# Kernel tuning notes

Hardware: AMD Instinct MI355X
Metric: run time of the kernel (lower is better)

Reference implementation:

```python
import jax, jax.numpy as jnp
import numpy as np

N = 50000
E = 800000
F_IN = 256
HID = 96
N_CLS = 32
NEG_SLOPE = 0.2


def setup_inputs() -> dict:
    key = jax.random.key(0)
    ks = jax.random.split(key, 10)
    x = jax.random.normal(ks[0], (N, F_IN), dtype=jnp.float32)
    edge_index = jax.random.randint(ks[1], (2, E), 0, N, dtype=jnp.int64)
    s1 = 1.0 / np.sqrt(F_IN)
    s2 = 1.0 / np.sqrt(HID)
    return {
        "x": x,
        "edge_index": edge_index,
        "W1": jax.random.normal(ks[2], (F_IN, HID), dtype=jnp.float32) * s1,
        "a1_src": jax.random.normal(ks[3], (HID,), dtype=jnp.float32) * s2,
        "a1_dst": jax.random.normal(ks[4], (HID,), dtype=jnp.float32) * s2,
        "b1": jnp.zeros((HID,), dtype=jnp.float32),
        "W2": jax.random.normal(ks[5], (HID, N_CLS), dtype=jnp.float32) * s2,
        "a2_src": jax.random.normal(ks[6], (N_CLS,), dtype=jnp.float32) * (1.0 / np.sqrt(N_CLS)),
        "a2_dst": jax.random.normal(ks[7], (N_CLS,), dtype=jnp.float32) * (1.0 / np.sqrt(N_CLS)),
        "b2": jnp.zeros((N_CLS,), dtype=jnp.float32),
    }


def _gat_conv(x, src, dst, W, a_src, a_dst, b, n_nodes):
    # single-head GATConv (PyG defaults), self-loops already in src/dst
    h = x @ W                                  # [N, out]
    alpha_src = h @ a_src                      # [N]
    alpha_dst = h @ a_dst                      # [N]
    e = alpha_src[src] + alpha_dst[dst]        # [E'] edge logits (msg j->i: dst groups)
    e = jnp.where(e > 0, e, NEG_SLOPE * e)     # leaky_relu
    # segment softmax over edges grouped by destination node
    m = jax.ops.segment_max(e, dst, num_segments=n_nodes)
    ex = jnp.exp(e - m[dst])
    denom = jax.ops.segment_sum(ex, dst, num_segments=n_nodes)
    alpha = ex / denom[dst]                    # [E']
    out = jax.ops.segment_sum(alpha[:, None] * h[src], dst, num_segments=n_nodes)
    return out + b


def reference(x, edge_index, W1, a1_src, a1_dst, b1, W2, a2_src, a2_dst, b2):
    loops = jnp.arange(N, dtype=edge_index.dtype)
    src = jnp.concatenate([edge_index[0], loops])
    dst = jnp.concatenate([edge_index[1], loops])
    h = _gat_conv(x, src, dst, W1, a1_src, a1_dst, b1, N)
    h = jax.nn.elu(h)
    # dropout omitted (eval mode, training=False)
    out = _gat_conv(h, src, dst, W2, a2_src, a2_dst, b2, N)
    return jax.nn.log_softmax(out, axis=1)
```

## Files before the change

kernel.cpp:

```cpp
#include <hip/hip_runtime.h>
#include <cstdint>
#include <cstddef>

#define NNODES 50000
#define NEDGES 800000
#define MEDGES (NEDGES + NNODES)
#define FIN    256
#define HID    96
#define NCLS   32
#define NEG_SLOPE 0.2f

#define NBUCK  391
#define BCAP   3072

typedef unsigned int uint32;
typedef __attribute__((ext_vector_type(8))) short short8;
typedef __attribute__((ext_vector_type(4))) float f32x4;

__device__ __forceinline__ ushort bf_round(float f) {
    uint32 u = __float_as_uint(f);
    u += 0x7FFFu + ((u >> 16) & 1u);
    return (ushort)(u >> 16);
}
__device__ __forceinline__ uint32 pack_bf16x2(float a, float b) {
    return (uint32)bf_round(a) | ((uint32)bf_round(b) << 16);
}
__device__ __forceinline__ float bf_lo(uint32 u) { return __uint_as_float(u << 16); }
__device__ __forceinline__ float bf_hi(uint32 u) { return __uint_as_float(u & 0xFFFF0000u); }
__device__ __forceinline__ float lrelu(float t) { return (t > 0.f) ? t : NEG_SLOPE * t; }
__device__ __forceinline__ float af(int i) { return __int_as_float(i); }
__device__ __forceinline__ float elu_fast(float t) { return (t > 0.f) ? t : (__expf(t) - 1.f); }


__global__ __launch_bounds__(256) void bucket1_kernel(const int* __restrict__ ei,
                                                      int* __restrict__ gcount,
                                                      int* __restrict__ staging) {
    __shared__ int hist[NBUCK];
    __shared__ int base_sh[NBUCK];
    for (int i = threadIdx.x; i < NBUCK; i += 256) hist[i] = 0;
    __syncthreads();

    int v[8], rk[8], bk[8];
    int e0 = blockIdx.x * 2048;
#pragma unroll
    for (int i = 0; i < 8; ++i) {
        int e = e0 + i * 256 + threadIdx.x;
        if (e < MEDGES) {
            int s, d;
            if (e < NEDGES) { s = ei[e]; d = ei[NEDGES + e]; }
            else            { s = e - NEDGES; d = s; }
            bk[i] = d >> 7;
            v[i]  = s | ((d & 127) << 16);
            rk[i] = atomicAdd(&hist[bk[i]], 1);
        } else bk[i] = -1;
    }
    __syncthreads();
    for (int i = threadIdx.x; i < NBUCK; i += 256) {
        int c = hist[i];
        base_sh[i] = c ? atomicAdd(&gcount[i], c) : 0;
    }
    __syncthreads();
#pragma unroll
    for (int i = 0; i < 8; ++i) {
        if (bk[i] >= 0) {
            int pos = base_sh[bk[i]] + rk[i];
            if (pos < BCAP)
                staging[(size_t)bk[i] * BCAP + pos] = v[i];
        }
    }
}

__global__ __launch_bounds__(256) void bucket2_kernel(const int* __restrict__ staging,
                                                      const int* __restrict__ gcount,
                                                      int* __restrict__ rowptr,
                                                      int* __restrict__ esrc) {
    __shared__ int dcount[128];
    __shared__ int dincl[128];
    __shared__ int dexcl[128];
    __shared__ int fillc[128];
    __shared__ int red_s[256];

    const int b = blockIdx.x;
    const int t = threadIdx.x;

    int pv = 0;
    for (int idx = t; idx < b; idx += 256) pv += gcount[idx];
    red_s[t] = pv;
    __syncthreads();
    for (int off2 = 128; off2; off2 >>= 1) {
        if (t < off2) red_s[t] += red_s[t + off2];
        __syncthreads();
    }
    const int ebase = red_s[0];
    const int cnt   = gcount[b];
    const int node0 = b << 7;
    const int* st   = staging + (size_t)b * BCAP;

    for (int i = t; i < 128; i += 256) { dcount[i] = 0; fillc[i] = 0; }
    __syncthreads();

    for (int i = t; i < cnt; i += 256)
        atomicAdd(&dcount[st[i] >> 16], 1);
    __syncthreads();

    if (t < 128) dincl[t] = dcount[t];
    __syncthreads();
    for (int off = 1; off < 128; off <<= 1) {
        int val = (t >= off && t < 128) ? dincl[t - off] : 0;
        __syncthreads();
        if (t < 128) dincl[t] += val;
        __syncthreads();
    }
    if (t < 128) {
        int excl = dincl[t] - dcount[t];
        dexcl[t] = excl;
        int node = node0 + t;
        if (node < NNODES) rowptr[node] = ebase + excl;
    }
    if (b == NBUCK - 1 && t == 0) rowptr[NNODES] = MEDGES;
    __syncthreads();

    for (int i = t; i < cnt; i += 256) {
        int v = st[i];
        int dd = v >> 16;
        int r = atomicAdd(&fillc[dd], 1);
        esrc[ebase + dexcl[dd] + r] = v & 0xFFFF;
    }
}


__global__ __launch_bounds__(256) void packw_kernel(const float* __restrict__ W1,
                                                    const float* __restrict__ W2,
                                                    ushort* __restrict__ W1p,
                                                    ushort* __restrict__ W2p,
                                                    int* __restrict__ gcount) {
    int stride = gridDim.x * 256;
    for (int idx = blockIdx.x * 256 + threadIdx.x; idx < NBUCK; idx += stride)
        gcount[idx] = 0;
    for (int idx = blockIdx.x * 256 + threadIdx.x; idx < 6 * 8 * 64 * 8; idx += stride) {
        int j     = idx & 7;
        int lane  = (idx >> 3) & 63;
        int kstep = (idx >> 9) & 7;
        int ntile = idx >> 12;
        int k = kstep * 32 + ((lane >> 4) << 3) + j;
        int n = ntile * 16 + (lane & 15);
        W1p[idx] = bf_round(W1[(size_t)k * 96 + n]);
    }
    for (int idx = blockIdx.x * 256 + threadIdx.x; idx < 2 * 3 * 64 * 8; idx += stride) {
        int j     = idx & 7;
        int lane  = (idx >> 3) & 63;
        int kstep = (idx >> 9) % 3;
        int ntile = (idx >> 9) / 3;
        int k = kstep * 32 + ((lane >> 4) << 3) + j;
        int n = ntile * 16 + (lane & 15);
        W2p[idx] = bf_round(W2[(size_t)k * 32 + n]);
    }
}


__global__ __launch_bounds__(256) void gemm1_kernel(const float* __restrict__ x,
                                                    const ushort* __restrict__ W1p,
                                                    const float* __restrict__ a_src,
                                                    const float* __restrict__ a_dst,
                                                    ushort* __restrict__ h1,
                                                    float* __restrict__ as1,
                                                    float* __restrict__ ad1) {
    const int tid  = threadIdx.x;
    const int lane = tid & 63;
    const int wv   = tid >> 6;
    const int m    = lane & 15;
    const int quad = lane >> 4;
    const int node0 = blockIdx.x * 64;

    int arow = node0 + wv * 16 + m;
    if (arow >= NNODES) arow = NNODES - 1;
    const float* xr = x + (size_t)arow * FIN + quad * 8;

    const short8* Wp = (const short8*)W1p;

    f32x4 acc[6];
#pragma unroll
    for (int t = 0; t < 6; ++t) acc[t] = (f32x4){0.f, 0.f, 0.f, 0.f};

#pragma unroll
    for (int ks = 0; ks < 8; ++ks) {
        float4 v0 = *(const float4*)(xr + ks * 32);
        float4 v1 = *(const float4*)(xr + ks * 32 + 4);
        short8 a;
        a[0] = (short)bf_round(v0.x); a[1] = (short)bf_round(v0.y);
        a[2] = (short)bf_round(v0.z); a[3] = (short)bf_round(v0.w);
        a[4] = (short)bf_round(v1.x); a[5] = (short)bf_round(v1.y);
        a[6] = (short)bf_round(v1.z); a[7] = (short)bf_round(v1.w);
#pragma unroll
        for (int t = 0; t < 6; ++t) {
            short8 b = Wp[(t * 8 + ks) * 64 + lane];
            acc[t] = __builtin_amdgcn_mfma_f32_16x16x32_bf16(a, b, acc[t], 0, 0, 0);
        }
    }

    float as_reg[6], ad_reg[6];
#pragma unroll
    for (int t = 0; t < 6; ++t) {
        as_reg[t] = a_src[t * 16 + m];
        ad_reg[t] = a_dst[t * 16 + m];
    }

#pragma unroll
    for (int r = 0; r < 4; ++r) {
        int node = node0 + wv * 16 + quad * 4 + r;
        float ps = 0.f, pd = 0.f;
#pragma unroll
        for (int t = 0; t < 6; ++t) {
            ps += acc[t][r] * as_reg[t];
            pd += acc[t][r] * ad_reg[t];
        }
#pragma unroll
        for (int off = 1; off < 16; off <<= 1) {
            ps += __shfl_xor(ps, off);
            pd += __shfl_xor(pd, off);
        }
        if (node < NNODES) {
            ushort* hp = h1 + (size_t)node * 96 + m;
#pragma unroll
            for (int t = 0; t < 6; ++t) hp[t * 16] = bf_round(acc[t][r]);
            if (m == 0) { as1[node] = ps; ad1[node] = pd; }
        }
    }
}


__global__ __launch_bounds__(256) void gemm2_kernel(const uint32* __restrict__ y48,
                                                    const ushort* __restrict__ W2p,
                                                    const float* __restrict__ a_src,
                                                    const float* __restrict__ a_dst,
                                                    uint32* __restrict__ h2b,
                                                    float* __restrict__ as2,
                                                    float* __restrict__ ad2) {
    const int tid  = threadIdx.x;
    const int lane = tid & 63;
    const int wv   = tid >> 6;
    const int m    = lane & 15;
    const int quad = lane >> 4;
    const int node0 = blockIdx.x * 64;

    int arow = node0 + wv * 16 + m;
    if (arow >= NNODES) arow = NNODES - 1;
    const short8* Ar = (const short8*)(y48 + (size_t)arow * 48);
    const short8* Wp = (const short8*)W2p;

    f32x4 acc[2];
    acc[0] = (f32x4){0.f, 0.f, 0.f, 0.f};
    acc[1] = (f32x4){0.f, 0.f, 0.f, 0.f};

#pragma unroll
    for (int ks = 0; ks < 3; ++ks) {
        short8 a = Ar[ks * 4 + quad];
#pragma unroll
        for (int t = 0; t < 2; ++t) {
            short8 b = Wp[(t * 3 + ks) * 64 + lane];
            acc[t] = __builtin_amdgcn_mfma_f32_16x16x32_bf16(a, b, acc[t], 0, 0, 0);
        }
    }

    float as_reg[2], ad_reg[2];
#pragma unroll
    for (int t = 0; t < 2; ++t) {
        as_reg[t] = a_src[t * 16 + m];
        ad_reg[t] = a_dst[t * 16 + m];
    }

#pragma unroll
    for (int r = 0; r < 4; ++r) {
        int node = node0 + wv * 16 + quad * 4 + r;
        float ps = 0.f, pd = 0.f;
#pragma unroll
        for (int t = 0; t < 2; ++t) {
            ps += acc[t][r] * as_reg[t];
            pd += acc[t][r] * ad_reg[t];
        }
#pragma unroll
        for (int off = 1; off < 16; off <<= 1) {
            ps += __shfl_xor(ps, off);
            pd += __shfl_xor(pd, off);
        }
        if (node < NNODES) {
            h2b[(size_t)node * 16 + m] = pack_bf16x2(acc[0][r], acc[1][r]);
            if (m == 0) { as2[node] = ps; ad2[node] = pd; }
        }
    }
}


__global__ __launch_bounds__(256) void agg96_kernel(const ushort* __restrict__ h,
                                                    const float* __restrict__ asrc,
                                                    const float* __restrict__ adst,
                                                    const float* __restrict__ bias,
                                                    const int* __restrict__ rowptr,
                                                    const int* __restrict__ esrc,
                                                    uint32* __restrict__ out1b) {
    __shared__ int2 sa[4][2][32];
    const int wave = threadIdx.x >> 6;
    const int lane = threadIdx.x & 63;
    const int hf   = lane >> 5;
    const int fl32 = lane & 31;
    const int i = blockIdx.x * 8 + wave * 2 + hf;

    const int start = rowptr[i];
    const int deg   = rowptr[i + 1] - start;
    const float ad  = adst[i];
    const int fl    = (fl32 < 24) ? fl32 : 23;

    float acc0 = 0.f, acc1 = 0.f, acc2 = 0.f, acc3 = 0.f;

    if (deg <= 32) {
        bool valid = fl32 < deg;
        int s_reg = valid ? esrc[start + fl32] : 0;
        float e = valid ? lrelu(asrc[s_reg] + ad) : -1e30f;
        float mx = e;
#pragma unroll
        for (int off = 16; off; off >>= 1) mx = fmaxf(mx, __shfl_xor(mx, off));
        float ex = valid ? __expf(e - mx) : 0.f;
        float sum = ex;
#pragma unroll
        for (int off = 16; off; off >>= 1) sum += __shfl_xor(sum, off);
        sa[wave][hf][fl32] = make_int2(s_reg, __float_as_int(ex / sum));

        const int4* sap = (const int4*)&sa[wave][hf][0];

        for (int eb = 0; eb < deg; eb += 8) {
            int4 qa = sap[(eb >> 1) + 0];
            int4 qb = sap[(eb >> 1) + 1];
            int4 qc = sap[(eb >> 1) + 2];
            int4 qd = sap[(eb >> 1) + 3];
            const uint2* r0 = (const uint2*)(h + (size_t)qa.x * 96);
            const uint2* r1 = (const uint2*)(h + (size_t)qa.z * 96);
            const uint2* r2 = (const uint2*)(h + (size_t)qb.x * 96);
            const uint2* r3 = (const uint2*)(h + (size_t)qb.z * 96);
            const uint2* r4 = (const uint2*)(h + (size_t)qc.x * 96);
            const uint2* r5 = (const uint2*)(h + (size_t)qc.z * 96);
            const uint2* r6 = (const uint2*)(h + (size_t)qd.x * 96);
            const uint2* r7 = (const uint2*)(h + (size_t)qd.z * 96);
            uint2 u0 = r0[fl], u1 = r1[fl], u2 = r2[fl], u3 = r3[fl];
            uint2 u4 = r4[fl], u5 = r5[fl], u6 = r6[fl], u7 = r7[fl];
            float a0 = af(qa.y), a1 = af(qa.w), a2 = af(qb.y), a3 = af(qb.w);
            float a4 = af(qc.y), a5 = af(qc.w), a6 = af(qd.y), a7 = af(qd.w);
            acc0 += a0 * bf_lo(u0.x) + a1 * bf_lo(u1.x) + a2 * bf_lo(u2.x) + a3 * bf_lo(u3.x)
                  + a4 * bf_lo(u4.x) + a5 * bf_lo(u5.x) + a6 * bf_lo(u6.x) + a7 * bf_lo(u7.x);
            acc1 += a0 * bf_hi(u0.x) + a1 * bf_hi(u1.x) + a2 * bf_hi(u2.x) + a3 * bf_hi(u3.x)
                  + a4 * bf_hi(u4.x) + a5 * bf_hi(u5.x) + a6 * bf_hi(u6.x) + a7 * bf_hi(u7.x);
            acc2 += a0 * bf_lo(u0.y) + a1 * bf_lo(u1.y) + a2 * bf_lo(u2.y) + a3 * bf_lo(u3.y)
                  + a4 * bf_lo(u4.y) + a5 * bf_lo(u5.y) + a6 * bf_lo(u6.y) + a7 * bf_lo(u7.y);
            acc3 += a0 * bf_hi(u0.y) + a1 * bf_hi(u1.y) + a2 * bf_hi(u2.y) + a3 * bf_hi(u3.y)
                  + a4 * bf_hi(u4.y) + a5 * bf_hi(u5.y) + a6 * bf_hi(u6.y) + a7 * bf_hi(u7.y);
        }
    } else {
        float mx = -1e30f;
        for (int p = start + fl32; p < start + deg; p += 32)
            mx = fmaxf(mx, lrelu(asrc[esrc[p]] + ad));
#pragma unroll
        for (int off = 16; off; off >>= 1) mx = fmaxf(mx, __shfl_xor(mx, off));
        float sum = 0.f;
        for (int p = start + fl32; p < start + deg; p += 32)
            sum += __expf(lrelu(asrc[esrc[p]] + ad) - mx);
#pragma unroll
        for (int off = 16; off; off >>= 1) sum += __shfl_xor(sum, off);
        float inv = 1.f / sum;
        for (int e = 0; e < deg; ++e) {
            int s = esrc[start + e];
            float a = __expf(lrelu(asrc[s] + ad) - mx) * inv;
            uint2 u = ((const uint2*)(h + (size_t)s * 96))[fl];
            acc0 += a * bf_lo(u.x);
            acc1 += a * bf_hi(u.x);
            acc2 += a * bf_lo(u.y);
            acc3 += a * bf_hi(u.y);
        }
    }

    if (fl32 < 24) {
        float v0 = elu_fast(acc0 + bias[4 * fl32 + 0]);
        float v1 = elu_fast(acc1 + bias[4 * fl32 + 1]);
        float v2 = elu_fast(acc2 + bias[4 * fl32 + 2]);
        float v3 = elu_fast(acc3 + bias[4 * fl32 + 3]);
        uint2 o;
        o.x = pack_bf16x2(v0, v1);
        o.y = pack_bf16x2(v2, v3);
        *(uint2*)(out1b + (size_t)i * 48 + 2 * fl32) = o;
    }
}


__global__ __launch_bounds__(256) void agg32_kernel(const uint32* __restrict__ h2b,
                                                    const float* __restrict__ asrc,
                                                    const float* __restrict__ adst,
                                                    const float* __restrict__ bias,
                                                    const int* __restrict__ rowptr,
                                                    const int* __restrict__ esrc,
                                                    float* __restrict__ out) {
    __shared__ int2 sa[4][2][32];
    const int wave = threadIdx.x >> 6;
    const int lane = threadIdx.x & 63;
    const int hf   = lane >> 5;
    const int fl32 = lane & 31;
    const int i = blockIdx.x * 8 + wave * 2 + hf;

    const int start = rowptr[i];
    const int deg   = rowptr[i + 1] - start;
    const float ad  = adst[i];
    const int g  = fl32 >> 3;
    const int fl = fl32 & 7;

    float acc[4];
#pragma unroll
    for (int j = 0; j < 4; ++j) acc[j] = 0.f;

    if (deg <= 32) {
        bool valid = fl32 < deg;
        int s_reg = valid ? esrc[start + fl32] : 0;
        float e = valid ? lrelu(asrc[s_reg] + ad) : -1e30f;
        float mx = e;
#pragma unroll
        for (int off = 16; off; off >>= 1) mx = fmaxf(mx, __shfl_xor(mx, off));
        float ex = valid ? __expf(e - mx) : 0.f;
        float sum = ex;
#pragma unroll
        for (int off = 16; off; off >>= 1) sum += __shfl_xor(sum, off);
        sa[wave][hf][fl32] = make_int2(s_reg, __float_as_int(ex / sum));

#pragma unroll 2
        for (int eb = 0; eb < deg; eb += 4) {
            int e0 = eb + g;
            int2 q = sa[wave][hf][(e0 < 32) ? e0 : 31];
            float a = (e0 < deg) ? af(q.y) : 0.f;
            const uint2* hr = (const uint2*)(h2b + (size_t)q.x * 16);
            uint2 u = hr[fl];
            acc[0] = fmaf(a, bf_lo(u.x), acc[0]);
            acc[1] = fmaf(a, bf_hi(u.x), acc[1]);
            acc[2] = fmaf(a, bf_lo(u.y), acc[2]);
            acc[3] = fmaf(a, bf_hi(u.y), acc[3]);
        }
    } else {
        float mx = -1e30f;
        for (int p = start + fl32; p < start + deg; p += 32)
            mx = fmaxf(mx, lrelu(asrc[esrc[p]] + ad));
#pragma unroll
        for (int off = 16; off; off >>= 1) mx = fmaxf(mx, __shfl_xor(mx, off));
        float sum = 0.f;
        for (int p = start + fl32; p < start + deg; p += 32)
            sum += __expf(lrelu(asrc[esrc[p]] + ad) - mx);
#pragma unroll
        for (int off = 16; off; off >>= 1) sum += __shfl_xor(sum, off);
        float inv = 1.f / sum;
        for (int p = start + g; p < start + deg; p += 4) {
            int s = esrc[p];
            float a = __expf(lrelu(asrc[s] + ad) - mx) * inv;
            const uint2* hr = (const uint2*)(h2b + (size_t)s * 16);
            uint2 u = hr[fl];
            acc[0] = fmaf(a, bf_lo(u.x), acc[0]);
            acc[1] = fmaf(a, bf_hi(u.x), acc[1]);
            acc[2] = fmaf(a, bf_lo(u.y), acc[2]);
            acc[3] = fmaf(a, bf_hi(u.y), acc[3]);
        }
    }

#pragma unroll
    for (int j = 0; j < 4; ++j) {
        acc[j] += __shfl_xor(acc[j], 8);
        acc[j] += __shfl_xor(acc[j], 16);
    }

    float z0 = acc[0] + bias[2 * fl];
    float z1 = acc[1] + bias[2 * fl + 16];
    float z2 = acc[2] + bias[2 * fl + 1];
    float z3 = acc[3] + bias[2 * fl + 17];
    float m2 = fmaxf(fmaxf(z0, z1), fmaxf(z2, z3));
#pragma unroll
    for (int off = 4; off; off >>= 1) m2 = fmaxf(m2, __shfl_xor(m2, off));
    float s2 = __expf(z0 - m2) + __expf(z1 - m2) + __expf(z2 - m2) + __expf(z3 - m2);
#pragma unroll
    for (int off = 4; off; off >>= 1) s2 += __shfl_xor(s2, off);
    float ls = m2 + __logf(s2);
    if (fl32 < 8) {
        float* op = out + (size_t)i * 32;
        op[2 * fl]      = z0 - ls;
        op[2 * fl + 16] = z1 - ls;
        op[2 * fl + 1]  = z2 - ls;
        op[2 * fl + 17] = z3 - ls;
    }
}


extern "C" void kernel_launch(void* const* d_in, const int* in_sizes, int n_in,
                              void* d_out, int out_size, void* d_ws, size_t ws_size,
                              hipStream_t stream) {
    const float* x   = (const float*)d_in[0];
    const int*   ei  = (const int*)d_in[1];
    const float* W1  = (const float*)d_in[2];
    const float* a1s = (const float*)d_in[3];
    const float* a1d = (const float*)d_in[4];
    const float* b1  = (const float*)d_in[5];
    const float* W2  = (const float*)d_in[6];
    const float* a2s = (const float*)d_in[7];
    const float* a2d = (const float*)d_in[8];
    const float* b2  = (const float*)d_in[9];
    float* out = (float*)d_out;

    size_t off = 0;
    auto alloc = [&](size_t bytes) {
        void* p = (char*)d_ws + off;
        off += (bytes + 255) & ~(size_t)255;
        return p;
    };
    ushort* h1    = (ushort*)alloc((size_t)NNODES * HID * 2);
    uint32* out1b = (uint32*)alloc((size_t)NNODES * 48 * 4);
    int*  staging = (int*)alloc((size_t)NBUCK * BCAP * 4);
    float* as1    = (float*)alloc((size_t)NNODES * 4);
    float* ad1    = (float*)alloc((size_t)NNODES * 4);
    float* as2    = (float*)alloc((size_t)NNODES * 4);
    float* ad2    = (float*)alloc((size_t)NNODES * 4);
    int*   rowptr = (int*)alloc((size_t)(NNODES + 1) * 4);
    int*   esrc   = (int*)alloc((size_t)MEDGES * 4);
    ushort* W1p   = (ushort*)alloc((size_t)6 * 8 * 64 * 8 * 2);
    ushort* W2p   = (ushort*)alloc((size_t)2 * 3 * 64 * 8 * 2);
    int*   gcount = (int*)alloc((size_t)NBUCK * 4);
    uint32* h2b   = (uint32*)h1;

    const int nbB1    = (MEDGES + 2047) / 2048;
    const int nbGemm  = (NNODES + 63) / 64;
    const int nbAggP  = NNODES / 8;

    packw_kernel<<<13, 256, 0, stream>>>(W1, W2, W1p, W2p, gcount);
    bucket1_kernel<<<nbB1, 256, 0, stream>>>(ei, gcount, staging);
    bucket2_kernel<<<NBUCK, 256, 0, stream>>>(staging, gcount, rowptr, esrc);

    gemm1_kernel<<<nbGemm, 256, 0, stream>>>(x, W1p, a1s, a1d, h1, as1, ad1);
    agg96_kernel<<<nbAggP, 256, 0, stream>>>(h1, as1, ad1, b1, rowptr, esrc, out1b);

    gemm2_kernel<<<nbGemm, 256, 0, stream>>>(out1b, W2p, a2s, a2d, h2b, as2, ad2);
    agg32_kernel<<<nbAggP, 256, 0, stream>>>(h2b, as2, ad2, b2, rowptr, esrc, out);
}
```

Before: 207.4 us.

## Fuse CSR bucket pass into GEMM1 launch and layer-2 GEMM into aggregation

The second bucketing pass and the first-layer GEMM become one launch, with block IDs split between the two independent jobs so they run concurrently. The layer-1 aggregation now finishes each node's ELU output in shared memory and does the 96x32 second-layer projection and its attention logits in FP32 right there. This removes the separate gemm2 kernel, the W2 packing and the round trip of the bf16 hidden activations through global memory. In exchange every aggregation block loads and transposes W2 into shared memory and does scalar FMAs instead of MFMA, and shared-memory use grows, which may lower occupancy.

```diff
diff --git a/kernel.cpp b/kernel.cpp
--- a/kernel.cpp
+++ b/kernel.cpp
@@ -32,107 +32,8 @@
 __device__ __forceinline__ float elu_fast(float t) { return (t > 0.f) ? t : (__expf(t) - 1.f); }
 
 
-__global__ __launch_bounds__(256) void bucket1_kernel(const int* __restrict__ ei,
-                                                      int* __restrict__ gcount,
-                                                      int* __restrict__ staging) {
-    __shared__ int hist[NBUCK];
-    __shared__ int base_sh[NBUCK];
-    for (int i = threadIdx.x; i < NBUCK; i += 256) hist[i] = 0;
-    __syncthreads();
-
-    int v[8], rk[8], bk[8];
-    int e0 = blockIdx.x * 2048;
-#pragma unroll
-    for (int i = 0; i < 8; ++i) {
-        int e = e0 + i * 256 + threadIdx.x;
-        if (e < MEDGES) {
-            int s, d;
-            if (e < NEDGES) { s = ei[e]; d = ei[NEDGES + e]; }
-            else            { s = e - NEDGES; d = s; }
-            bk[i] = d >> 7;
-            v[i]  = s | ((d & 127) << 16);
-            rk[i] = atomicAdd(&hist[bk[i]], 1);
-        } else bk[i] = -1;
-    }
-    __syncthreads();
-    for (int i = threadIdx.x; i < NBUCK; i += 256) {
-        int c = hist[i];
-        base_sh[i] = c ? atomicAdd(&gcount[i], c) : 0;
-    }
-    __syncthreads();
-#pragma unroll
-    for (int i = 0; i < 8; ++i) {
-        if (bk[i] >= 0) {
-            int pos = base_sh[bk[i]] + rk[i];
-            if (pos < BCAP)
-                staging[(size_t)bk[i] * BCAP + pos] = v[i];
-        }
-    }
-}
-
-__global__ __launch_bounds__(256) void bucket2_kernel(const int* __restrict__ staging,
-                                                      const int* __restrict__ gcount,
-                                                      int* __restrict__ rowptr,
-                                                      int* __restrict__ esrc) {
-    __shared__ int dcount[128];
-    __shared__ int dincl[128];
-    __shared__ int dexcl[128];
-    __shared__ int fillc[128];
-    __shared__ int red_s[256];
-
-    const int b = blockIdx.x;
-    const int t = threadIdx.x;
-
-    int pv = 0;
-    for (int idx = t; idx < b; idx += 256) pv += gcount[idx];
-    red_s[t] = pv;
-    __syncthreads();
-    for (int off2 = 128; off2; off2 >>= 1) {
-        if (t < off2) red_s[t] += red_s[t + off2];
-        __syncthreads();
-    }
-    const int ebase = red_s[0];
-    const int cnt   = gcount[b];
-    const int node0 = b << 7;
-    const int* st   = staging + (size_t)b * BCAP;
-
-    for (int i = t; i < 128; i += 256) { dcount[i] = 0; fillc[i] = 0; }
-    __syncthreads();
-
-    for (int i = t; i < cnt; i += 256)
-        atomicAdd(&dcount[st[i] >> 16], 1);
-    __syncthreads();
-
-    if (t < 128) dincl[t] = dcount[t];
-    __syncthreads();
-    for (int off = 1; off < 128; off <<= 1) {
-        int val = (t >= off && t < 128) ? dincl[t - off] : 0;
-        __syncthreads();
-        if (t < 128) dincl[t] += val;
-        __syncthreads();
-    }
-    if (t < 128) {
-        int excl = dincl[t] - dcount[t];
-        dexcl[t] = excl;
-        int node = node0 + t;
-        if (node < NNODES) rowptr[node] = ebase + excl;
-    }
-    if (b == NBUCK - 1 && t == 0) rowptr[NNODES] = MEDGES;
-    __syncthreads();
-
-    for (int i = t; i < cnt; i += 256) {
-        int v = st[i];
-        int dd = v >> 16;
-        int r = atomicAdd(&fillc[dd], 1);
-        esrc[ebase + dexcl[dd] + r] = v & 0xFFFF;
-    }
-}
-
-
 __global__ __launch_bounds__(256) void packw_kernel(const float* __restrict__ W1,
-                                                    const float* __restrict__ W2,
                                                     ushort* __restrict__ W1p,
-                                                    ushort* __restrict__ W2p,
                                                     int* __restrict__ gcount) {
     int stride = gridDim.x * 256;
     for (int idx = blockIdx.x * 256 + threadIdx.x; idx < NBUCK; idx += stride)
@@ -146,31 +47,121 @@
         int n = ntile * 16 + (lane & 15);
         W1p[idx] = bf_round(W1[(size_t)k * 96 + n]);
     }
-    for (int idx = blockIdx.x * 256 + threadIdx.x; idx < 2 * 3 * 64 * 8; idx += stride) {
-        int j     = idx & 7;
-        int lane  = (idx >> 3) & 63;
-        int kstep = (idx >> 9) % 3;
-        int ntile = (idx >> 9) / 3;
-        int k = kstep * 32 + ((lane >> 4) << 3) + j;
-        int n = ntile * 16 + (lane & 15);
-        W2p[idx] = bf_round(W2[(size_t)k * 32 + n]);
-    }
-}
-
-
-__global__ __launch_bounds__(256) void gemm1_kernel(const float* __restrict__ x,
-                                                    const ushort* __restrict__ W1p,
-                                                    const float* __restrict__ a_src,
-                                                    const float* __restrict__ a_dst,
-                                                    ushort* __restrict__ h1,
-                                                    float* __restrict__ as1,
-                                                    float* __restrict__ ad1) {
+}
+
+
+__global__ __launch_bounds__(256) void bucket1_kernel(const int* __restrict__ ei,
+                                                      int* __restrict__ gcount,
+                                                      int* __restrict__ staging) {
+    __shared__ int hist[NBUCK];
+    __shared__ int base_sh[NBUCK];
+    for (int i = threadIdx.x; i < NBUCK; i += 256) hist[i] = 0;
+    __syncthreads();
+
+    int v[8], rk[8], bk[8];
+    int e0 = blockIdx.x * 2048;
+#pragma unroll
+    for (int i = 0; i < 8; ++i) {
+        int e = e0 + i * 256 + threadIdx.x;
+        if (e < MEDGES) {
+            int s, d;
+            if (e < NEDGES) { s = ei[e]; d = ei[NEDGES + e]; }
+            else            { s = e - NEDGES; d = s; }
+            bk[i] = d >> 7;
+            v[i]  = s | ((d & 127) << 16);
+            rk[i] = atomicAdd(&hist[bk[i]], 1);
+        } else bk[i] = -1;
+    }
+    __syncthreads();
+    for (int i = threadIdx.x; i < NBUCK; i += 256) {
+        int c = hist[i];
+        base_sh[i] = c ? atomicAdd(&gcount[i], c) : 0;
+    }
+    __syncthreads();
+#pragma unroll
+    for (int i = 0; i < 8; ++i) {
+        if (bk[i] >= 0) {
+            int pos = base_sh[bk[i]] + rk[i];
+            if (pos < BCAP)
+                staging[(size_t)bk[i] * BCAP + pos] = v[i];
+        }
+    }
+}
+
+
+__global__ __launch_bounds__(256) void b2gemm1_kernel(const int* __restrict__ staging,
+                                                      const int* __restrict__ gcount,
+                                                      int* __restrict__ rowptr,
+                                                      int* __restrict__ esrc,
+                                                      const float* __restrict__ x,
+                                                      const ushort* __restrict__ W1p,
+                                                      const float* __restrict__ a_src,
+                                                      const float* __restrict__ a_dst,
+                                                      ushort* __restrict__ h1,
+                                                      float* __restrict__ as1,
+                                                      float* __restrict__ ad1) {
+    __shared__ int dcount[128];
+    __shared__ int dincl[128];
+    __shared__ int dexcl[128];
+    __shared__ int fillc[128];
+    __shared__ int red_s[256];
+
+    if (blockIdx.x < NBUCK) {
+        const int b = blockIdx.x;
+        const int t = threadIdx.x;
+
+        int pv = 0;
+        for (int idx = t; idx < b; idx += 256) pv += gcount[idx];
+        red_s[t] = pv;
+        __syncthreads();
+        for (int off2 = 128; off2; off2 >>= 1) {
+            if (t < off2) red_s[t] += red_s[t + off2];
+            __syncthreads();
+        }
+        const int ebase = red_s[0];
+        const int cnt   = gcount[b];
+        const int node0 = b << 7;
+        const int* st   = staging + (size_t)b * BCAP;
+
+        for (int i = t; i < 128; i += 256) { dcount[i] = 0; fillc[i] = 0; }
+        __syncthreads();
+
+        for (int i = t; i < cnt; i += 256)
+            atomicAdd(&dcount[st[i] >> 16], 1);
+        __syncthreads();
+
+        if (t < 128) dincl[t] = dcount[t];
+        __syncthreads();
+        for (int off = 1; off < 128; off <<= 1) {
+            int val = (t >= off && t < 128) ? dincl[t - off] : 0;
+            __syncthreads();
+            if (t < 128) dincl[t] += val;
+            __syncthreads();
+        }
+        if (t < 128) {
+            int excl = dincl[t] - dcount[t];
+            dexcl[t] = excl;
+            int node = node0 + t;
+            if (node < NNODES) rowptr[node] = ebase + excl;
+        }
+        if (b == NBUCK - 1 && t == 0) rowptr[NNODES] = MEDGES;
+        __syncthreads();
+
+        for (int i = t; i < cnt; i += 256) {
+            int v = st[i];
+            int dd = v >> 16;
+            int r = atomicAdd(&fillc[dd], 1);
+            esrc[ebase + dexcl[dd] + r] = v & 0xFFFF;
+        }
+        return;
+    }
+
     const int tid  = threadIdx.x;
     const int lane = tid & 63;
     const int wv   = tid >> 6;
     const int m    = lane & 15;
     const int quad = lane >> 4;
-    const int node0 = blockIdx.x * 64;
+    const int node0 = (blockIdx.x - NBUCK) * 64;
 
     int arow = node0 + wv * 16 + m;
     if (arow >= NNODES) arow = NNODES - 1;
@@ -229,76 +220,28 @@
 }
 
 
-__global__ __launch_bounds__(256) void gemm2_kernel(const uint32* __restrict__ y48,
-                                                    const ushort* __restrict__ W2p,
-                                                    const float* __restrict__ a_src,
-                                                    const float* __restrict__ a_dst,
-                                                    uint32* __restrict__ h2b,
-                                                    float* __restrict__ as2,
-                                                    float* __restrict__ ad2) {
-    const int tid  = threadIdx.x;
-    const int lane = tid & 63;
-    const int wv   = tid >> 6;
-    const int m    = lane & 15;
-    const int quad = lane >> 4;
-    const int node0 = blockIdx.x * 64;
-
-    int arow = node0 + wv * 16 + m;
-    if (arow >= NNODES) arow = NNODES - 1;
-    const short8* Ar = (const short8*)(y48 + (size_t)arow * 48);
-    const short8* Wp = (const short8*)W2p;
-
-    f32x4 acc[2];
-    acc[0] = (f32x4){0.f, 0.f, 0.f, 0.f};
-    acc[1] = (f32x4){0.f, 0.f, 0.f, 0.f};
-
-#pragma unroll
-    for (int ks = 0; ks < 3; ++ks) {
-        short8 a = Ar[ks * 4 + quad];
-#pragma unroll
-        for (int t = 0; t < 2; ++t) {
-            short8 b = Wp[(t * 3 + ks) * 64 + lane];
-            acc[t] = __builtin_amdgcn_mfma_f32_16x16x32_bf16(a, b, acc[t], 0, 0, 0);
-        }
-    }
-
-    float as_reg[2], ad_reg[2];
-#pragma unroll
-    for (int t = 0; t < 2; ++t) {
-        as_reg[t] = a_src[t * 16 + m];
-        ad_reg[t] = a_dst[t * 16 + m];
-    }
-
-#pragma unroll
-    for (int r = 0; r < 4; ++r) {
-        int node = node0 + wv * 16 + quad * 4 + r;
-        float ps = 0.f, pd = 0.f;
-#pragma unroll
-        for (int t = 0; t < 2; ++t) {
-            ps += acc[t][r] * as_reg[t];
-            pd += acc[t][r] * ad_reg[t];
-        }
-#pragma unroll
-        for (int off = 1; off < 16; off <<= 1) {
-            ps += __shfl_xor(ps, off);
-            pd += __shfl_xor(pd, off);
-        }
-        if (node < NNODES) {
-            h2b[(size_t)node * 16 + m] = pack_bf16x2(acc[0][r], acc[1][r]);
-            if (m == 0) { as2[node] = ps; ad2[node] = pd; }
-        }
-    }
-}
-
-
-__global__ __launch_bounds__(256) void agg96_kernel(const ushort* __restrict__ h,
-                                                    const float* __restrict__ asrc,
-                                                    const float* __restrict__ adst,
-                                                    const float* __restrict__ bias,
-                                                    const int* __restrict__ rowptr,
-                                                    const int* __restrict__ esrc,
-                                                    uint32* __restrict__ out1b) {
+__global__ __launch_bounds__(256) void agg96g2_kernel(const ushort* __restrict__ h,
+                                                      const float* __restrict__ asrc,
+                                                      const float* __restrict__ adst,
+                                                      const float* __restrict__ bias,
+                                                      const int* __restrict__ rowptr,
+                                                      const int* __restrict__ esrc,
+                                                      const float* __restrict__ W2,
+                                                      const float* __restrict__ a2s,
+                                                      const float* __restrict__ a2d,
+                                                      uint32* __restrict__ h2b,
+                                                      float* __restrict__ as2,
+                                                      float* __restrict__ ad2) {
     __shared__ int2 sa[4][2][32];
+    __shared__ __align__(16) float W2t[32 * 100];
+    __shared__ __align__(16) float y_sh[4][2][96];
+
+    for (int idx = threadIdx.x; idx < 96 * 32; idx += 256) {
+        int c = idx & 31, k = idx >> 5;
+        W2t[c * 100 + k] = W2[idx];
+    }
+    __syncthreads();
+
     const int wave = threadIdx.x >> 6;
     const int lane = threadIdx.x & 63;
     const int hf   = lane >> 5;
@@ -308,6 +251,8 @@
     const int start = rowptr[i];
     const int deg   = rowptr[i + 1] - start;
     const float ad  = adst[i];
+    const float a2s_v = a2s[fl32];
+    const float a2d_v = a2d[fl32];
     const int fl    = (fl32 < 24) ? fl32 : 23;
 
     float acc0 = 0.f, acc1 = 0.f, acc2 = 0.f, acc3 = 0.f;
@@ -377,15 +322,38 @@
     }
 
     if (fl32 < 24) {
-        float v0 = elu_fast(acc0 + bias[4 * fl32 + 0]);
-        float v1 = elu_fast(acc1 + bias[4 * fl32 + 1]);
-        float v2 = elu_fast(acc2 + bias[4 * fl32 + 2]);
-        float v3 = elu_fast(acc3 + bias[4 * fl32 + 3]);
-        uint2 o;
-        o.x = pack_bf16x2(v0, v1);
-        o.y = pack_bf16x2(v2, v3);
-        *(uint2*)(out1b + (size_t)i * 48 + 2 * fl32) = o;
-    }
+        float* yp = &y_sh[wave][hf][4 * fl32];
+        yp[0] = elu_fast(acc0 + bias[4 * fl32 + 0]);
+        yp[1] = elu_fast(acc1 + bias[4 * fl32 + 1]);
+        yp[2] = elu_fast(acc2 + bias[4 * fl32 + 2]);
+        yp[3] = elu_fast(acc3 + bias[4 * fl32 + 3]);
+    }
+    asm volatile("s_waitcnt lgkmcnt(0)" ::: "memory");
+
+    const float* yrow = &y_sh[wave][hf][0];
+    const float* wcol = W2t + fl32 * 100;
+    float h2c = 0.f;
+#pragma unroll
+    for (int k = 0; k < 96; k += 4) {
+        float4 yv = *(const float4*)(yrow + k);
+        float4 wv = *(const float4*)(wcol + k);
+        h2c = fmaf(yv.x, wv.x, h2c);
+        h2c = fmaf(yv.y, wv.y, h2c);
+        h2c = fmaf(yv.z, wv.z, h2c);
+        h2c = fmaf(yv.w, wv.w, h2c);
+    }
+
+    float ps = h2c * a2s_v;
+    float pd = h2c * a2d_v;
+#pragma unroll
+    for (int off = 1; off < 32; off <<= 1) {
+        ps += __shfl_xor(ps, off);
+        pd += __shfl_xor(pd, off);
+    }
+    float partner = __shfl_xor(h2c, 16);
+    if (fl32 < 16)
+        h2b[(size_t)i * 16 + fl32] = pack_bf16x2(h2c, partner);
+    if (fl32 == 0) { as2[i] = ps; ad2[i] = pd; }
 }
 
 
@@ -511,7 +479,7 @@
         return p;
     };
     ushort* h1    = (ushort*)alloc((size_t)NNODES * HID * 2);
-    uint32* out1b = (uint32*)alloc((size_t)NNODES * 48 * 4);
+    uint32* h2b   = (uint32*)alloc((size_t)NNODES * 16 * 4);
     int*  staging = (int*)alloc((size_t)NBUCK * BCAP * 4);
     float* as1    = (float*)alloc((size_t)NNODES * 4);
     float* ad1    = (float*)alloc((size_t)NNODES * 4);
@@ -520,21 +488,17 @@
     int*   rowptr = (int*)alloc((size_t)(NNODES + 1) * 4);
     int*   esrc   = (int*)alloc((size_t)MEDGES * 4);
     ushort* W1p   = (ushort*)alloc((size_t)6 * 8 * 64 * 8 * 2);
-    ushort* W2p   = (ushort*)alloc((size_t)2 * 3 * 64 * 8 * 2);
     int*   gcount = (int*)alloc((size_t)NBUCK * 4);
-    uint32* h2b   = (uint32*)h1;
 
     const int nbB1    = (MEDGES + 2047) / 2048;
     const int nbGemm  = (NNODES + 63) / 64;
     const int nbAggP  = NNODES / 8;
 
-    packw_kernel<<<13, 256, 0, stream>>>(W1, W2, W1p, W2p, gcount);
+    packw_kernel<<<16, 256, 0, stream>>>(W1, W1p, gcount);
     bucket1_kernel<<<nbB1, 256, 0, stream>>>(ei, gcount, staging);
-    bucket2_kernel<<<NBUCK, 256, 0, stream>>>(staging, gcount, rowptr, esrc);
-
-    gemm1_kernel<<<nbGemm, 256, 0, stream>>>(x, W1p, a1s, a1d, h1, as1, ad1);
-    agg96_kernel<<<nbAggP, 256, 0, stream>>>(h1, as1, ad1, b1, rowptr, esrc, out1b);
-
-    gemm2_kernel<<<nbGemm, 256, 0, stream>>>(out1b, W2p, a2s, a2d, h2b, as2, ad2);
+    b2gemm1_kernel<<<NBUCK + nbGemm, 256, 0, stream>>>(staging, gcount, rowptr, esrc,
+                                                       x, W1p, a1s, a1d, h1, as1, ad1);
+    agg96g2_kernel<<<nbAggP, 256, 0, stream>>>(h1, as1, ad1, b1, rowptr, esrc,
+                                               W2, a2s, a2d, h2b, as2, ad2);
     agg32_kernel<<<nbAggP, 256, 0, stream>>>(h2b, as2, ad2, b2, rowptr, esrc, out);
 }
```

Result: no change. 207.4 us (+0.0%).
